# Performance work log

Measured on AMD Instinct MI355X. Metric: run time of the kernel, lower is better.

The kernel has to match this reference:

```python
import jax, jax.numpy as jnp
import numpy as np

D_MODEL, N_HEAD, N_KV_HEAD, D_HEAD = 1024, 16, 4, 64


def rotate_half(x):
    x1, x2 = x[..., : x.shape[-1] // 2], x[..., x.shape[-1] // 2:]
    return jnp.concatenate((-x2, x1), axis=-1)


def rope_cos_sin(seq_len, dim, dtype=jnp.float32):
    inv_freq = 1.0 / (10000.0 ** (jnp.arange(0, dim, 2, dtype=jnp.float32) / dim))
    t = jnp.arange(seq_len, dtype=jnp.float32)
    freqs = jnp.einsum('i,j->ij', t, inv_freq)          # [S, dim/2]
    emb = jnp.concatenate((freqs, freqs), axis=-1)       # [S, dim]
    return jnp.cos(emb).astype(dtype), jnp.sin(emb).astype(dtype)


def setup_inputs() -> dict:
    key = jax.random.key(0)
    ks = jax.random.split(key, 5)
    B, S = 2, 2048
    scale = 0.02
    return {
        'x': jax.random.normal(ks[0], (B, S, D_MODEL), dtype=jnp.float32),
        'Wq': jax.random.normal(ks[1], (D_MODEL, N_HEAD * D_HEAD), dtype=jnp.float32) * scale,
        'Wk': jax.random.normal(ks[2], (D_MODEL, N_KV_HEAD * D_HEAD), dtype=jnp.float32) * scale,
        'Wv': jax.random.normal(ks[3], (D_MODEL, N_KV_HEAD * D_HEAD), dtype=jnp.float32) * scale,
        'Wo': jax.random.normal(ks[4], (N_HEAD * D_HEAD, D_MODEL), dtype=jnp.float32) * scale,
    }


def reference(x, Wq, Wk, Wv, Wo):
    B, S, _ = x.shape
    scale = 1.0 / np.sqrt(D_HEAD)
    # projections -> [B, H, S, Dh]
    q = (x @ Wq).reshape(B, S, N_HEAD, D_HEAD).transpose(0, 2, 1, 3)
    k = (x @ Wk).reshape(B, S, N_KV_HEAD, D_HEAD).transpose(0, 2, 1, 3)
    v = (x @ Wv).reshape(B, S, N_KV_HEAD, D_HEAD).transpose(0, 2, 1, 3)
    cos, sin = rope_cos_sin(S, D_HEAD, x.dtype)          # [S, Dh]
    q = q * cos + rotate_half(q) * sin
    k = k * cos + rotate_half(k) * sin
    rep = N_HEAD // N_KV_HEAD
    k = jnp.repeat(k, rep, axis=1)                       # [B, H, S, Dh]
    v = jnp.repeat(v, rep, axis=1)
    scores = jnp.einsum('bhqd,bhkd->bhqk', q, k) * scale # [B, H, S, S]
    causal = jnp.triu(jnp.ones((S, S), dtype=bool), k=1)
    scores = jnp.where(causal, -jnp.inf, scores)
    probs = jax.nn.softmax(scores, axis=-1)
    ctx = jnp.einsum('bhqk,bhkd->bhqd', probs, v)        # [B, H, S, Dh]
    ctx = ctx.transpose(0, 2, 1, 3).reshape(B, S, N_HEAD * D_HEAD)
    return ctx @ Wo
```

## Files before the change

kernel.cpp:

```cpp
#include <hip/hip_runtime.h>
#include <hip/hip_bf16.h>
#include <cstdint>
#include <math.h>

#define S_LEN 2048
#define DM 1024
#define NQKV 1536
#define MROWS 4096

typedef __attribute__((ext_vector_type(8))) short short8;
typedef __attribute__((ext_vector_type(4))) short short4v;
typedef __attribute__((ext_vector_type(4))) float f32x4;

#define MEMBAR() __asm__ __volatile__("" ::: "memory")

#define QFOLD 0.18033688011112042f

__device__ __forceinline__ short f2bf(float x) {
  union { float f; uint32_t u; } v; v.f = x;
  uint32_t r = (v.u + 0x7fffu + ((v.u >> 16) & 1u)) >> 16;
  return (short)(uint16_t)r;
}

__device__ __forceinline__ uint32_t pk2(float a, float b) {
  __hip_bfloat162 h = __float22bfloat162_rn(make_float2(a, b));
  union { __hip_bfloat162 h2; uint32_t u; } cv; cv.h2 = h;
  return cv.u;
}

__global__ void f32_to_bf16_vec(const float* __restrict__ in, short* __restrict__ out, int n4) {
  int i = blockIdx.x * blockDim.x + threadIdx.x;
  if (i < n4) {
    float4 v = ((const float4*)in)[i];
    short4 o;
    o.x = f2bf(v.x); o.y = f2bf(v.y); o.z = f2bf(v.z); o.w = f2bf(v.w);
    ((short4*)out)[i] = o;
  }
}

__global__ __launch_bounds__(256) void transpose_f32_bf16(const float* __restrict__ src,
    short* __restrict__ dst, int R, int C) {
  __shared__ short T[64 * 72];
  const int r0 = blockIdx.x * 64, c0 = blockIdx.y * 64;
  const int tid = threadIdx.x;
  #pragma unroll
  for (int i = 0; i < 4; ++i) {
    int chunk = tid + i * 256;
    int r = chunk >> 4, cc = (chunk & 15) * 4;
    float4 v = *(const float4*)&src[(size_t)(r0 + r) * C + c0 + cc];
    T[(cc + 0) * 72 + r] = f2bf(v.x);
    T[(cc + 1) * 72 + r] = f2bf(v.y);
    T[(cc + 2) * 72 + r] = f2bf(v.z);
    T[(cc + 3) * 72 + r] = f2bf(v.w);
  }
  __syncthreads();
  #pragma unroll
  for (int i = 0; i < 2; ++i) {
    int chunk = tid + i * 256;
    int rr = chunk >> 3, kk = (chunk & 7) * 8;
    *(uint4*)&dst[(size_t)(c0 + rr) * R + r0 + kk] = *(uint4*)&T[rr * 72 + kk];
  }
}

#define BM 128
#define BN 128
#define BKT 64

__global__ __launch_bounds__(256) void gemm_bf16(const short* __restrict__ A,
    const short* __restrict__ BT, float* __restrict__ C, int M, int N, int K) {
  __shared__ short As[BM * BKT];
  __shared__ short Bs[BN * BKT];
  const int tid = threadIdx.x;
  const int wave = tid >> 6, lane = tid & 63;
  const int quad = lane >> 4, l15 = lane & 15;
  const int wm = (wave >> 1) * 64, wn = (wave & 1) * 64;
  const int m0 = blockIdx.y * BM, n0 = blockIdx.x * BN;

  const int sr = wave * 32 + (lane >> 3);
  const int scol = (lane & 7) * 8;

  f32x4 acc[4][4] = {};

  for (int k0 = 0; k0 < K; k0 += BKT) {
    __syncthreads();
    #pragma unroll
    for (int j = 0; j < 4; ++j) {
      const int r = sr + j * 8;
      __builtin_amdgcn_global_load_lds(
          (const __attribute__((address_space(1))) void*)&A[(size_t)(m0 + r) * K + k0 + scol],
          (__attribute__((address_space(3))) void*)&As[(wave * 4 + j) * 512],
          16, 0, 0);
      __builtin_amdgcn_global_load_lds(
          (const __attribute__((address_space(1))) void*)&BT[(size_t)(n0 + r) * K + k0 + scol],
          (__attribute__((address_space(3))) void*)&Bs[(wave * 4 + j) * 512],
          16, 0, 0);
    }
    __syncthreads();
    #pragma unroll
    for (int ks = 0; ks < 2; ++ks) {
      short8 af[4], bfr[4];
      #pragma unroll
      for (int mi = 0; mi < 4; ++mi)
        af[mi] = *(const short8*)&As[(wm + mi*16 + l15)*BKT + ks*32 + quad*8];
      #pragma unroll
      for (int ni = 0; ni < 4; ++ni)
        bfr[ni] = *(const short8*)&Bs[(wn + ni*16 + l15)*BKT + ks*32 + quad*8];
      #pragma unroll
      for (int mi = 0; mi < 4; ++mi)
        #pragma unroll
        for (int ni = 0; ni < 4; ++ni)
          acc[mi][ni] = __builtin_amdgcn_mfma_f32_16x16x32_bf16(af[mi], bfr[ni], acc[mi][ni], 0, 0, 0);
    }
  }
  #pragma unroll
  for (int mi = 0; mi < 4; ++mi)
    #pragma unroll
    for (int ni = 0; ni < 4; ++ni)
      #pragma unroll
      for (int r = 0; r < 4; ++r)
        C[(size_t)(m0 + wm + mi*16 + quad*4 + r)*N + (n0 + wn + ni*16 + l15)] = acc[mi][ni][r];
}

__global__ void rope_kernel(const float* __restrict__ qkv, short* __restrict__ Qb,
                            short* __restrict__ Kb, short* __restrict__ Vb) {
  __shared__ float csn[64];
  const int row = blockIdx.x;
  const int s = row & (S_LEN - 1);
  const int tid = threadIdx.x;
  const float* rp = qkv + (size_t)row * NQKV;
  if (tid < 32) {
    float inv = exp2f(-(float)tid * 0.41524101186092029f);
    float ang = (float)s * inv;
    csn[tid] = cosf(ang);
    csn[tid + 32] = sinf(ang);
  }
  __syncthreads();
  #pragma unroll
  for (int i = 0; i < 2; ++i) {
    int p = tid + i * 256;
    int hh = p >> 5, j = p & 31;
    float cs = csn[j], sn = csn[j + 32];
    float x1 = rp[hh*64 + j], x2 = rp[hh*64 + j + 32];
    Qb[(size_t)row*1024 + hh*64 + j]      = f2bf((x1*cs - x2*sn) * QFOLD);
    Qb[(size_t)row*1024 + hh*64 + j + 32] = f2bf((x2*cs + x1*sn) * QFOLD);
  }
  if (tid < 128) {
    int hh = tid >> 5, j = tid & 31;
    float cs = csn[j], sn = csn[j + 32];
    float x1 = rp[1024 + hh*64 + j], x2 = rp[1024 + hh*64 + j + 32];
    Kb[(size_t)row*256 + hh*64 + j]      = f2bf(x1*cs - x2*sn);
    Kb[(size_t)row*256 + hh*64 + j + 32] = f2bf(x2*cs + x1*sn);
  }
  Vb[(size_t)row*256 + tid] = f2bf(rp[1280 + tid]);
}

__global__ __launch_bounds__(256) void transpose_v(const short* __restrict__ Vb,
                                                   short* __restrict__ Vt) {
  __shared__ short T[64 * 72];
  const int s0 = blockIdx.x * 64;
  const int bh = blockIdx.y;
  const int b = bh >> 2, kvh = bh & 3;
  const int tid = threadIdx.x;
  #pragma unroll
  for (int i = 0; i < 2; ++i) {
    int chunk = tid + i * 256;
    int r = chunk >> 3, c = (chunk & 7) * 8;
    short8 v = *(const short8*)&Vb[(size_t)(b*S_LEN + s0 + r)*256 + kvh*64 + c];
    #pragma unroll
    for (int t = 0; t < 8; ++t) T[(c + t) * 72 + r] = v[t];
  }
  __syncthreads();
  #pragma unroll
  for (int i = 0; i < 2; ++i) {
    int chunk = tid + i * 256;
    int rr = chunk >> 3, kk = (chunk & 7) * 8;
    *(uint4*)&Vt[(size_t)(bh*64 + rr)*S_LEN + s0 + kk] = *(uint4*)&T[rr * 72 + kk];
  }
}

#define PSTR 136

__global__ __launch_bounds__(256, 2) void fattn6(const short* __restrict__ Qb,
    const short* __restrict__ Kb, const short* __restrict__ Vt, short* __restrict__ Ctx) {
  __shared__ short Ks[128 * 72];
  __shared__ short Vts[64 * PSTR];
  __shared__ short Ps[4 * 16 * PSTR];
  const int idx = blockIdx.x;
  const int pi  = idx & 15;
  const int h   = (idx >> 4) & 15;
  const int b   = idx >> 8;
  const int kvh = h >> 2;
  const int tid = threadIdx.x, wave = tid >> 6, lane = tid & 63;
  const int quad = lane >> 4, l15 = lane & 15;
  const int roff = wave * 16;
  const size_t qbase  = (size_t)b * S_LEN * 1024;
  const size_t kbase  = (size_t)b * S_LEN * 256;
  const size_t vtbase = (size_t)(b*4 + kvh) * 64 * S_LEN;
  short* Psw = Ps + wave * 16 * PSTR;

  for (int half = 0; half < 2; ++half) {
    const int jt = half ? (31 - pi) : pi;
    const int q0 = jt * 64;
    const int ntiles = (jt >> 1) + 1;
    const int qrow = q0 + roff + l15;

    const short* qp = &Qb[qbase + (size_t)(q0 + roff + l15)*1024 + h*64 + quad*8];
    short8 qf0 = *(const short8*)qp;
    short8 qf1 = *(const short8*)(qp + 32);

    f32x4 O[4] = {};
    float ll = 0.f;

    short8 kreg[4], vreg[4];
    #pragma unroll
    for (int i = 0; i < 4; ++i) {
      int chunk = tid + i * 256;
      int kr = chunk >> 3, kc = (chunk & 7) * 8;
      kreg[i] = *(const short8*)&Kb[kbase + (size_t)kr*256 + kvh*64 + kc];
      int vr = chunk >> 4, vc = (chunk & 15) * 8;
      vreg[i] = *(const short8*)&Vt[vtbase + (size_t)vr*S_LEN + vc];
    }

    for (int t = 0; t < ntiles; ++t) {
      const int k0 = t * 128;
      __syncthreads();
      #pragma unroll
      for (int i = 0; i < 4; ++i) {
        int chunk = tid + i * 256;
        int kr = chunk >> 3, kc = (chunk & 7) * 8;
        *(short8*)&Ks[kr*72 + kc] = kreg[i];
        int vr = chunk >> 4, vc = (chunk & 15) * 8;
        *(short8*)&Vts[vr*PSTR + vc] = vreg[i];
      }
      __syncthreads();
      if (t + 1 < ntiles) {
        const int kn = (t + 1) * 128;
        #pragma unroll
        for (int i = 0; i < 4; ++i) {
          int chunk = tid + i * 256;
          int kr = chunk >> 3, kc = (chunk & 7) * 8;
          kreg[i] = *(const short8*)&Kb[kbase + (size_t)(kn + kr)*256 + kvh*64 + kc];
          int vr = chunk >> 4, vc = (chunk & 15) * 8;
          vreg[i] = *(const short8*)&Vt[vtbase + (size_t)vr*S_LEN + kn + vc];
        }
      }

      f32x4 sc[8];
      #pragma unroll
      for (int nt = 0; nt < 8; ++nt) {
        short8 kf0 = *(const short8*)&Ks[(nt*16 + l15)*72 + quad*8];
        short8 kf1 = *(const short8*)&Ks[(nt*16 + l15)*72 + 32 + quad*8];
        f32x4 a = {0.f, 0.f, 0.f, 0.f};
        a = __builtin_amdgcn_mfma_f32_16x16x32_bf16(kf0, qf0, a, 0, 0, 0);
        a = __builtin_amdgcn_mfma_f32_16x16x32_bf16(kf1, qf1, a, 0, 0, 0);
        sc[nt] = a;
      }
      if (t == ntiles - 1) {
        #pragma unroll
        for (int nt = 0; nt < 8; ++nt)
          #pragma unroll
          for (int r = 0; r < 4; ++r)
            if (k0 + nt*16 + quad*4 + r > qrow) sc[nt][r] = -1e30f;
      }
      #pragma unroll
      for (int nt = 0; nt < 8; ++nt) {
        float p0 = exp2f(sc[nt][0]);
        float p1 = exp2f(sc[nt][1]);
        float p2 = exp2f(sc[nt][2]);
        float p3 = exp2f(sc[nt][3]);
        ll += (p0 + p1) + (p2 + p3);
        union { uint2 uu; short4v s; } pkc;
        pkc.uu.x = pk2(p0, p1); pkc.uu.y = pk2(p2, p3);
        *(short4v*)&Psw[l15*PSTR + nt*16 + quad*4] = pkc.s;
      }
      MEMBAR();
      #pragma unroll
      for (int ks = 0; ks < 4; ++ks) {
        short8 a = *(const short8*)&Psw[l15*PSTR + ks*32 + quad*8];
        #pragma unroll
        for (int d = 0; d < 4; ++d) {
          short8 bv = *(const short8*)&Vts[(d*16 + l15)*PSTR + ks*32 + quad*8];
          O[d] = __builtin_amdgcn_mfma_f32_16x16x32_bf16(a, bv, O[d], 0, 0, 0);
        }
      }
    }

    ll += __shfl_xor(ll, 16, 64);
    ll += __shfl_xor(ll, 32, 64);
    #pragma unroll
    for (int r = 0; r < 4; ++r) {
      float lr = __shfl(ll, quad*4 + r, 64);
      float inv = 1.0f / lr;
      #pragma unroll
      for (int d = 0; d < 4; ++d) {
        int qr = q0 + roff + quad*4 + r;
        Ctx[qbase + (size_t)qr*1024 + h*64 + d*16 + l15] = f2bf(O[d][r] * inv);
      }
    }
  }
}

extern "C" void kernel_launch(void* const* d_in, const int* in_sizes, int n_in,
                              void* d_out, int out_size, void* d_ws, size_t ws_size,
                              hipStream_t stream) {
  const float* x  = (const float*)d_in[0];
  const float* Wq = (const float*)d_in[1];
  const float* Wk = (const float*)d_in[2];
  const float* Wv = (const float*)d_in[3];
  const float* Wo = (const float*)d_in[4];
  float* out = (float*)d_out;

  char* w = (char*)d_ws;
  short* Xb    = (short*)w;  w += (size_t)MROWS * DM * 2;
  short* WcatT = (short*)w;  w += (size_t)NQKV * DM * 2;
  short* WoT   = (short*)w;  w += (size_t)DM * DM * 2;
  float* QKVf  = (float*)w;  w += (size_t)MROWS * NQKV * 4;
  short* Qbuf  = (short*)w;  w += (size_t)MROWS * DM * 2;
  short* Kbuf  = (short*)w;  w += (size_t)MROWS * 256 * 2;
  short* Vbuf  = (short*)w;  w += (size_t)MROWS * 256 * 2;
  short* Vt    = (short*)w;  w += (size_t)8 * 64 * S_LEN * 2;
  short* Ctx   = (short*)QKVf;

  f32_to_bf16_vec<<<dim3(4096), dim3(256), 0, stream>>>(x, Xb, MROWS * DM / 4);
  transpose_f32_bf16<<<dim3(16, 16), dim3(256), 0, stream>>>(Wq, WcatT, 1024, 1024);
  transpose_f32_bf16<<<dim3(16, 4),  dim3(256), 0, stream>>>(Wk, WcatT + (size_t)1024*1024, 1024, 256);
  transpose_f32_bf16<<<dim3(16, 4),  dim3(256), 0, stream>>>(Wv, WcatT + (size_t)1280*1024, 1024, 256);
  transpose_f32_bf16<<<dim3(16, 16), dim3(256), 0, stream>>>(Wo, WoT, 1024, 1024);

  gemm_bf16<<<dim3(NQKV / BN, MROWS / BM), dim3(256), 0, stream>>>(Xb, WcatT, QKVf, MROWS, NQKV, DM);
  rope_kernel<<<dim3(MROWS), dim3(256), 0, stream>>>(QKVf, Qbuf, Kbuf, Vbuf);
  transpose_v<<<dim3(32, 8), dim3(256), 0, stream>>>(Vbuf, Vt);
  fattn6<<<dim3(512), dim3(256), 0, stream>>>(Qbuf, Kbuf, Vt, Ctx);
  gemm_bf16<<<dim3(DM / BN, MROWS / BM), dim3(256), 0, stream>>>(Ctx, WoT, out, MROWS, DM, DM);
}
```

Measured before the change: 194.3 us.

## Rewrite attention with 32x32 MFMA, direct global-to-LDS double buffering, swizzled K/V

Replaces the 16x16 MFMA attention kernel with a 128-thread variant that uses 32x32x16 MFMAs, one 32-row query strip per wave. P stays in registers, rearranged with v_permlane32_swap, instead of going through LDS. K and V tiles are loaded straight into double-buffered LDS with global_load_lds. Producer kernels write K and Vt with an XOR swizzle so the unpadded LDS layout avoids bank conflicts. This removes the register-staged copies and the P round-trip through shared memory. In exchange, the smaller blocks and launch_bounds(128,1) may lower occupancy.

After: 207.0 us. 1.07x slower.

```diff
diff --git a/kernel.cpp b/kernel.cpp
--- a/kernel.cpp
+++ b/kernel.cpp
@@ -9,10 +9,8 @@
 #define MROWS 4096
 
 typedef __attribute__((ext_vector_type(8))) short short8;
-typedef __attribute__((ext_vector_type(4))) short short4v;
 typedef __attribute__((ext_vector_type(4))) float f32x4;
-
-#define MEMBAR() __asm__ __volatile__("" ::: "memory")
+typedef __attribute__((ext_vector_type(16))) float f32x16;
 
 #define QFOLD 0.18033688011112042f
 
@@ -148,8 +146,9 @@
     int hh = tid >> 5, j = tid & 31;
     float cs = csn[j], sn = csn[j + 32];
     float x1 = rp[1024 + hh*64 + j], x2 = rp[1024 + hh*64 + j + 32];
-    Kb[(size_t)row*256 + hh*64 + j]      = f2bf(x1*cs - x2*sn);
-    Kb[(size_t)row*256 + hh*64 + j + 32] = f2bf(x2*cs + x1*sn);
+    const int sw = (s & 7) << 3;
+    Kb[(size_t)row*256 + hh*64 + (j ^ sw)]        = f2bf(x1*cs - x2*sn);
+    Kb[(size_t)row*256 + hh*64 + ((j + 32) ^ sw)] = f2bf(x2*cs + x1*sn);
   }
   Vb[(size_t)row*256 + tid] = f2bf(rp[1280 + tid]);
 }
@@ -174,130 +173,142 @@
   for (int i = 0; i < 2; ++i) {
     int chunk = tid + i * 256;
     int rr = chunk >> 3, kk = (chunk & 7) * 8;
-    *(uint4*)&Vt[(size_t)(bh*64 + rr)*S_LEN + s0 + kk] = *(uint4*)&T[rr * 72 + kk];
-  }
-}
-
-#define PSTR 136
-
-__global__ __launch_bounds__(256, 2) void fattn6(const short* __restrict__ Qb,
+    *(uint4*)&Vt[(size_t)(bh*64 + rr)*S_LEN + s0 + (kk ^ ((rr & 7) << 3))] = *(uint4*)&T[rr * 72 + kk];
+  }
+}
+
+__global__ __launch_bounds__(128, 1) void fattn7(const short* __restrict__ Qb,
     const short* __restrict__ Kb, const short* __restrict__ Vt, short* __restrict__ Ctx) {
-  __shared__ short Ks[128 * 72];
-  __shared__ short Vts[64 * PSTR];
-  __shared__ short Ps[4 * 16 * PSTR];
+  __shared__ short Ks[2][128 * 64];
+  __shared__ short Vts[2][64 * 128];
   const int idx = blockIdx.x;
   const int pi  = idx & 15;
   const int h   = (idx >> 4) & 15;
   const int b   = idx >> 8;
   const int kvh = h >> 2;
-  const int tid = threadIdx.x, wave = tid >> 6, lane = tid & 63;
-  const int quad = lane >> 4, l15 = lane & 15;
-  const int roff = wave * 16;
+  const int tid = threadIdx.x, wav = tid >> 6, lane = tid & 63;
+  const int l31 = lane & 31, hi = lane >> 5;
   const size_t qbase  = (size_t)b * S_LEN * 1024;
   const size_t kbase  = (size_t)b * S_LEN * 256;
-  const size_t vtbase = (size_t)(b*4 + kvh) * 64 * S_LEN;
-  short* Psw = Ps + wave * 16 * PSTR;
+  const size_t vtbase = (size_t)(b * 4 + kvh) * 64 * S_LEN;
+
+  const short* kptr = Kb + kbase + (size_t)(wav * 8 + (lane >> 3)) * 256 + kvh * 64 + (lane & 7) * 8;
+  const short* vptr = Vt + vtbase + (size_t)(wav * 4 + (lane >> 4)) * 2048 + (lane & 15) * 8;
+
+#define STAGE(bi, k0s) do { \
+    const short* kp_ = kptr + (size_t)(k0s) * 256; \
+    const short* vp_ = vptr + (k0s); \
+    short* kd_ = &Ks[bi][wav * 512]; \
+    short* vd_ = &Vts[bi][wav * 512]; \
+    _Pragma("unroll") \
+    for (int i_ = 0; i_ < 8; ++i_) { \
+      __builtin_amdgcn_global_load_lds((const __attribute__((address_space(1))) void*)(kp_ + i_ * 4096), \
+          (__attribute__((address_space(3))) void*)(kd_ + i_ * 1024), 16, 0, 0); \
+      __builtin_amdgcn_global_load_lds((const __attribute__((address_space(1))) void*)(vp_ + i_ * 16384), \
+          (__attribute__((address_space(3))) void*)(vd_ + i_ * 1024), 16, 0, 0); \
+    } \
+  } while (0)
 
   for (int half = 0; half < 2; ++half) {
     const int jt = half ? (31 - pi) : pi;
     const int q0 = jt * 64;
     const int ntiles = (jt >> 1) + 1;
-    const int qrow = q0 + roff + l15;
-
-    const short* qp = &Qb[qbase + (size_t)(q0 + roff + l15)*1024 + h*64 + quad*8];
-    short8 qf0 = *(const short8*)qp;
-    short8 qf1 = *(const short8*)(qp + 32);
-
-    f32x4 O[4] = {};
-    float ll = 0.f;
-
-    short8 kreg[4], vreg[4];
-    #pragma unroll
-    for (int i = 0; i < 4; ++i) {
-      int chunk = tid + i * 256;
-      int kr = chunk >> 3, kc = (chunk & 7) * 8;
-      kreg[i] = *(const short8*)&Kb[kbase + (size_t)kr*256 + kvh*64 + kc];
-      int vr = chunk >> 4, vc = (chunk & 15) * 8;
-      vreg[i] = *(const short8*)&Vt[vtbase + (size_t)vr*S_LEN + vc];
-    }
+    const int qg = q0 + wav * 32 + l31;
+
+    short8 qf[4];
+    {
+      const short* qp = &Qb[qbase + (size_t)qg * 1024 + h * 64 + hi * 8];
+      #pragma unroll
+      for (int ks = 0; ks < 4; ++ks) qf[ks] = *(const short8*)(qp + ks * 16);
+    }
+
+    f32x16 O0 = {}, O1 = {};
+    float la0 = 0.f, la1 = 0.f, la2 = 0.f, la3 = 0.f;
+
+    STAGE(0, 0);
+    __syncthreads();
 
     for (int t = 0; t < ntiles; ++t) {
+      const int cur = t & 1;
       const int k0 = t * 128;
-      __syncthreads();
-      #pragma unroll
-      for (int i = 0; i < 4; ++i) {
-        int chunk = tid + i * 256;
-        int kr = chunk >> 3, kc = (chunk & 7) * 8;
-        *(short8*)&Ks[kr*72 + kc] = kreg[i];
-        int vr = chunk >> 4, vc = (chunk & 15) * 8;
-        *(short8*)&Vts[vr*PSTR + vc] = vreg[i];
+      if (t + 1 < ntiles) STAGE((t + 1) & 1, (t + 1) * 128);
+
+      const short* ks_ = Ks[cur];
+      const short* vs_ = Vts[cur];
+
+      f32x16 sc[4];
+      #pragma unroll
+      for (int kt = 0; kt < 4; ++kt) {
+        const int r = kt * 32 + l31;
+        const int rx = (r & 7) << 3;
+        f32x16 a = {};
+        #pragma unroll
+        for (int ks2 = 0; ks2 < 4; ++ks2) {
+          short8 kf = *(const short8*)&ks_[r * 64 + ((ks2 * 16 + hi * 8) ^ rx)];
+          a = __builtin_amdgcn_mfma_f32_32x32x16_bf16(kf, qf[ks2], a, 0, 0, 0);
+        }
+        sc[kt] = a;
       }
-      __syncthreads();
-      if (t + 1 < ntiles) {
-        const int kn = (t + 1) * 128;
-        #pragma unroll
-        for (int i = 0; i < 4; ++i) {
-          int chunk = tid + i * 256;
-          int kr = chunk >> 3, kc = (chunk & 7) * 8;
-          kreg[i] = *(const short8*)&Kb[kbase + (size_t)(kn + kr)*256 + kvh*64 + kc];
-          int vr = chunk >> 4, vc = (chunk & 15) * 8;
-          vreg[i] = *(const short8*)&Vt[vtbase + (size_t)vr*S_LEN + kn + vc];
+
+      if (t == ntiles - 1) {
+        #pragma unroll
+        for (int kt = 0; kt < 4; ++kt)
+          #pragma unroll
+          for (int r = 0; r < 16; ++r) {
+            const int kvg = k0 + kt * 32 + (r & 3) + 8 * (r >> 2) + 4 * hi;
+            if (kvg > qg) sc[kt][r] = -1e30f;
+          }
+      }
+
+      short8 af[8];
+      #pragma unroll
+      for (int kt = 0; kt < 4; ++kt) {
+        #pragma unroll
+        for (int r = 0; r < 16; ++r) sc[kt][r] = exp2f(sc[kt][r]);
+        la0 += (sc[kt][0] + sc[kt][1]) + (sc[kt][2] + sc[kt][3]);
+        la1 += (sc[kt][4] + sc[kt][5]) + (sc[kt][6] + sc[kt][7]);
+        la2 += (sc[kt][8] + sc[kt][9]) + (sc[kt][10] + sc[kt][11]);
+        la3 += (sc[kt][12] + sc[kt][13]) + (sc[kt][14] + sc[kt][15]);
+        #pragma unroll
+        for (int st = 0; st < 2; ++st) {
+          uint32_t x0 = pk2(sc[kt][st * 8 + 0], sc[kt][st * 8 + 1]);
+          uint32_t x1 = pk2(sc[kt][st * 8 + 2], sc[kt][st * 8 + 3]);
+          uint32_t x2 = pk2(sc[kt][st * 8 + 4], sc[kt][st * 8 + 5]);
+          uint32_t x3 = pk2(sc[kt][st * 8 + 6], sc[kt][st * 8 + 7]);
+          asm("v_permlane32_swap_b32 %0, %1" : "+v"(x0), "+v"(x2));
+          asm("v_permlane32_swap_b32 %0, %1" : "+v"(x1), "+v"(x3));
+          union { short8 s8; uint32_t u[4]; } cv;
+          cv.u[0] = x0; cv.u[1] = x1; cv.u[2] = x2; cv.u[3] = x3;
+          af[kt * 2 + st] = cv.s8;
         }
       }
 
-      f32x4 sc[8];
-      #pragma unroll
-      for (int nt = 0; nt < 8; ++nt) {
-        short8 kf0 = *(const short8*)&Ks[(nt*16 + l15)*72 + quad*8];
-        short8 kf1 = *(const short8*)&Ks[(nt*16 + l15)*72 + 32 + quad*8];
-        f32x4 a = {0.f, 0.f, 0.f, 0.f};
-        a = __builtin_amdgcn_mfma_f32_16x16x32_bf16(kf0, qf0, a, 0, 0, 0);
-        a = __builtin_amdgcn_mfma_f32_16x16x32_bf16(kf1, qf1, a, 0, 0, 0);
-        sc[nt] = a;
+      const int vx = (l31 & 7) << 3;
+      #pragma unroll
+      for (int s = 0; s < 8; ++s) {
+        const int co = s * 16 + hi * 8;
+        short8 bv0 = *(const short8*)&vs_[l31 * 128 + (co ^ vx)];
+        O0 = __builtin_amdgcn_mfma_f32_32x32x16_bf16(af[s], bv0, O0, 0, 0, 0);
+        short8 bv1 = *(const short8*)&vs_[(32 + l31) * 128 + (co ^ vx)];
+        O1 = __builtin_amdgcn_mfma_f32_32x32x16_bf16(af[s], bv1, O1, 0, 0, 0);
       }
-      if (t == ntiles - 1) {
-        #pragma unroll
-        for (int nt = 0; nt < 8; ++nt)
-          #pragma unroll
-          for (int r = 0; r < 4; ++r)
-            if (k0 + nt*16 + quad*4 + r > qrow) sc[nt][r] = -1e30f;
-      }
-      #pragma unroll
-      for (int nt = 0; nt < 8; ++nt) {
-        float p0 = exp2f(sc[nt][0]);
-        float p1 = exp2f(sc[nt][1]);
-        float p2 = exp2f(sc[nt][2]);
-        float p3 = exp2f(sc[nt][3]);
-        ll += (p0 + p1) + (p2 + p3);
-        union { uint2 uu; short4v s; } pkc;
-        pkc.uu.x = pk2(p0, p1); pkc.uu.y = pk2(p2, p3);
-        *(short4v*)&Psw[l15*PSTR + nt*16 + quad*4] = pkc.s;
-      }
-      MEMBAR();
-      #pragma unroll
-      for (int ks = 0; ks < 4; ++ks) {
-        short8 a = *(const short8*)&Psw[l15*PSTR + ks*32 + quad*8];
-        #pragma unroll
-        for (int d = 0; d < 4; ++d) {
-          short8 bv = *(const short8*)&Vts[(d*16 + l15)*PSTR + ks*32 + quad*8];
-          O[d] = __builtin_amdgcn_mfma_f32_16x16x32_bf16(a, bv, O[d], 0, 0, 0);
-        }
-      }
-    }
-
-    ll += __shfl_xor(ll, 16, 64);
+
+      __syncthreads();
+    }
+
+    float ll = (la0 + la1) + (la2 + la3);
     ll += __shfl_xor(ll, 32, 64);
-    #pragma unroll
-    for (int r = 0; r < 4; ++r) {
-      float lr = __shfl(ll, quad*4 + r, 64);
-      float inv = 1.0f / lr;
-      #pragma unroll
-      for (int d = 0; d < 4; ++d) {
-        int qr = q0 + roff + quad*4 + r;
-        Ctx[qbase + (size_t)qr*1024 + h*64 + d*16 + l15] = f2bf(O[d][r] * inv);
-      }
-    }
-  }
+    const float inv = 1.0f / ll;
+    #pragma unroll
+    for (int r = 0; r < 16; ++r) {
+      const int crow = (r & 3) + 8 * (r >> 2) + 4 * hi;
+      const float invr = __shfl(inv, crow, 64);
+      const size_t o = qbase + (size_t)(q0 + wav * 32 + crow) * 1024 + h * 64;
+      Ctx[o + l31]      = f2bf(O0[r] * invr);
+      Ctx[o + 32 + l31] = f2bf(O1[r] * invr);
+    }
+  }
+#undef STAGE
 }
 
 extern "C" void kernel_launch(void* const* d_in, const int* in_sizes, int n_in,
@@ -330,6 +341,6 @@
   gemm_bf16<<<dim3(NQKV / BN, MROWS / BM), dim3(256), 0, stream>>>(Xb, WcatT, QKVf, MROWS, NQKV, DM);
   rope_kernel<<<dim3(MROWS), dim3(256), 0, stream>>>(QKVf, Qbuf, Kbuf, Vbuf);
   transpose_v<<<dim3(32, 8), dim3(256), 0, stream>>>(Vbuf, Vt);
-  fattn6<<<dim3(512), dim3(256), 0, stream>>>(Qbuf, Kbuf, Vt, Ctx);
+  fattn7<<<dim3(512), dim3(128), 0, stream>>>(Qbuf, Kbuf, Vt, Ctx);
   gemm_bf16<<<dim3(DM / BN, MROWS / BM), dim3(256), 0, stream>>>(Ctx, WoT, out, MROWS, DM, DM);
 }
```
